# Kernel optimization log

Hardware: AMD Instinct MI355X
Metric: run time of the kernel (lower is better)

The kernel has to match this reference:

```python
import jax, jax.numpy as jnp
import numpy as np

EPS = 1e-12
B, C, H, M, E, P = 2, 20000, 64, 8, 200000, 3


def setup_inputs() -> dict:
    key = jax.random.key(0)
    ks = jax.random.split(key, 24)
    inp = {}
    inp["features"] = jax.random.normal(ks[0], (B, C, H), jnp.float32)
    inp["positions"] = jax.random.normal(ks[1], (B, C, P), jnp.float32)
    inp["edge_index"] = jax.random.randint(ks[2], (2, E), 0, C)
    inp["degree"] = jax.random.randint(ks[3], (C,), 1, 33).astype(jnp.float32)
    inp["cell_node_indices"] = jax.random.randint(ks[4], (C, M), 0, C)
    mask = (jax.random.uniform(ks[5], (C, M)) > 0.3).astype(jnp.float32)
    inp["cell_node_mask"] = mask.at[:, 0].set(1.0)  # first node always valid (pad semantics)

    def lin(k, fan_in, fan_out):
        return (jax.random.normal(k, (fan_in, fan_out), jnp.float32) / np.sqrt(fan_in)).astype(jnp.float32)

    # message MLP: Linear(2H+4 -> H), SiLU, Linear(H -> H)
    inp["W1"] = lin(ks[6], 2 * H + 4, H); inp["b1"] = jnp.zeros((H,), jnp.float32)
    inp["W2"] = lin(ks[7], H, H);         inp["b2"] = jnp.zeros((H,), jnp.float32)
    # position MLP: Linear(H -> H), SiLU, Linear(H -> 1)
    inp["P1"] = lin(ks[8], H, H);  inp["pb1"] = jnp.zeros((H,), jnp.float32)
    inp["P2"] = lin(ks[9], H, 1);  inp["pb2"] = jnp.zeros((1,), jnp.float32)
    # update MLP: Linear(2H -> H), SiLU, Linear(H -> H)
    inp["U1"] = lin(ks[10], 2 * H, H); inp["ub1"] = jnp.zeros((H,), jnp.float32)
    inp["U2"] = lin(ks[11], H, H);     inp["ub2"] = jnp.zeros((H,), jnp.float32)
    return inp


def _mlp(x, Wa, ba, Wb, bb):
    return jax.nn.silu(x @ Wa + ba) @ Wb + bb


def _forward(features, positions, edge_index, degree, cell_node_indices, cell_node_mask,
             W1, b1, W2, b2, P1, pb1, P2, pb2, U1, ub1, U2, ub2):
    src, dst = edge_index[0], edge_index[1]
    # gather padded node positions per cell: [B, C, M, P]
    node_pos = positions[:, cell_node_indices]

    h_src = features[:, src]                      # [B,E,H]
    h_dst = features[:, dst]
    rel = positions[:, src] - positions[:, dst]   # [B,E,P]
    dist = jnp.linalg.norm(rel, axis=-1, keepdims=True)  # [B,E,1]

    sp = node_pos[:, src]                         # [B,E,M,P]
    dp = node_pos[:, dst]
    mx = cell_node_mask[src]                      # [E,M]
    my = cell_node_mask[dst]

    # pairwise distances [B,E,M,M] via gram trick (avoids [B,E,M,M,P] intermediate)
    sp2 = jnp.sum(sp * sp, -1)                    # [B,E,M]
    dp2 = jnp.sum(dp * dp, -1)
    cross = jnp.einsum('bemp,benp->bemn', sp, dp)
    d = jnp.sqrt(jnp.maximum(sp2[..., :, None] + dp2[..., None, :] - 2.0 * cross, 0.0) + EPS)

    # masked pairwise-distance sum
    w = mx[:, :, None] * my[:, None, :]           # [E,M,M]
    pairwise = jnp.sum(d * w[None], axis=(-1, -2))  # [B,E]

    # centroid distance
    denx = jnp.maximum(mx.sum(-1, keepdims=True), EPS)  # [E,1]
    deny = jnp.maximum(my.sum(-1, keepdims=True), EPS)
    cx = jnp.sum(sp * mx[None, :, :, None], axis=2) / denx[None]  # [B,E,P]
    cy = jnp.sum(dp * my[None, :, :, None], axis=2) / deny[None]
    centroid = jnp.linalg.norm(cx - cy, axis=-1)  # [B,E]

    # Hausdorff distance (masked min/max)
    inf = jnp.float32(jnp.inf)
    d_xy = jnp.where(my[None, :, None, :] <= 0, inf, d)
    min_xy = jnp.where(mx[None] <= 0, 0.0, d_xy.min(-1))  # [B,E,M]
    h_xy = min_xy.max(-1)                                  # [B,E]
    d_yx = jnp.where(mx[None, :, None, :] <= 0, inf, jnp.swapaxes(d, -1, -2))
    min_yx = jnp.where(my[None] <= 0, 0.0, d_yx.min(-1))
    h_yx = min_yx.max(-1)
    haus = jnp.maximum(h_xy, h_yx)

    invariants = jnp.concatenate([dist, pairwise[..., None], centroid[..., None], haus[..., None]], -1)  # [B,E,4]
    msg_in = jnp.concatenate([h_src, h_dst, invariants], -1)  # [B,E,2H+4]
    messages = _mlp(msg_in, W1, b1, W2, b2)                   # [B,E,H]

    # scatter-aggregate into destination cells, degree-normalize
    agg = jnp.zeros_like(features).at[:, dst].add(messages)
    agg = agg / jnp.maximum(degree, 1.0)[None, :, None]

    # position update
    wts = jnp.tanh(_mlp(messages, P1, pb1, P2, pb2))          # [B,E,1]
    pos_upd = jnp.zeros_like(positions).at[:, dst].add(wts * rel)

    new_features = features + _mlp(jnp.concatenate([features, agg], -1), U1, ub1, U2, ub2)
    new_positions = positions + pos_upd
    return new_features, new_positions


def reference(features, positions, edge_index, degree, cell_node_indices, cell_node_mask,
              W1, b1, W2, b2, P1, pb1, P2, pb2, U1, ub1, U2, ub2):
    return _forward(features, positions, edge_index, degree, cell_node_indices, cell_node_mask,
                    W1, b1, W2, b2, P1, pb1, P2, pb2, U1, ub1, U2, ub2)
```

## Files before the change

### kernel.cpp

```cpp
#include <hip/hip_runtime.h>
#include <hip/hip_bf16.h>

#define B_ 2
#define C_ 20000
#define H_ 64
#define M_ 8
#define E_ 200000
#define P_ 3
#define EPS_ 1e-12f
#define ET_ (E_ / 64)

typedef __attribute__((ext_vector_type(8))) short short8;
typedef __attribute__((ext_vector_type(4))) float float4v;

__device__ __forceinline__ float rcp_(float x)  { return __builtin_amdgcn_rcpf(x); }
__device__ __forceinline__ float sqrt_(float x) { return __builtin_amdgcn_sqrtf(x); }
__device__ __forceinline__ float silu_(float x) {
    return x * __builtin_amdgcn_rcpf(1.f + __expf(-x));
}
__device__ __forceinline__ float tanh_(float x) {
    float e = __expf(2.f * x);
    return 1.f - 2.f * __builtin_amdgcn_rcpf(e + 1.f);
}
__device__ __forceinline__ unsigned short f2b(float f) {
    unsigned u = __float_as_uint(f);
    unsigned r = (u + 0x7FFF + ((u >> 16) & 1)) >> 16;
    return (unsigned short)r;
}
__device__ __forceinline__ float b2f(unsigned short h) {
    return __uint_as_float(((unsigned)h) << 16);
}
__device__ __forceinline__ unsigned pk2u(float a, float b) {
    __hip_bfloat162 h = __float22bfloat162_rn(make_float2(a, b));
    unsigned u; __builtin_memcpy(&u, &h, sizeof(u)); return u;
}
__device__ __forceinline__ float lo16f(unsigned u) { return __uint_as_float(u << 16); }
__device__ __forceinline__ float hi16f(unsigned u) { return __uint_as_float(u & 0xFFFF0000u); }

#define W1S_OFF 0
#define W2S_OFF 8192
#define P1S_OFF 12288
#define U1S_OFF 16384
#define U2S_OFF 24576
#define WBUF_ELEMS 28672

#define NB_PREP  120
#define NB_FEATB 2500
#define NB_DESC  157
#define NB_HIST  782
#define NB_ZAGG  2500
#define NB_PCOPY 118
#define NB_COMBO (NB_PREP + NB_FEATB + NB_DESC + NB_HIST + NB_ZAGG + NB_PCOPY)


__global__ __launch_bounds__(256) void combo_kernel(
    const float* __restrict__ W1, const float* __restrict__ W2,
    const float* __restrict__ P1, const float* __restrict__ U1,
    const float* __restrict__ U2, unsigned short* __restrict__ wbuf,
    const float* __restrict__ feat, unsigned short* __restrict__ featb,
    const float* __restrict__ pos, const int* __restrict__ cni,
    const float* __restrict__ mask, unsigned* __restrict__ descp,
    const int* __restrict__ ei, int* __restrict__ cnt,
    float* __restrict__ aggf, float* __restrict__ out_pos)
{
    const int bid = blockIdx.x;
    if (bid < NB_PREP) {
        int t = bid * 256 + threadIdx.x;
        if (t >= WBUF_ELEMS) return;
        const float* W; int e;
        if (t < W2S_OFF)      { W = W1; e = t; }
        else if (t < U1S_OFF) { W = (t < P1S_OFF) ? W2 : P1; e = (t < P1S_OFF) ? t - W2S_OFF : t - P1S_OFF; }
        else if (t < U2S_OFF) { W = U1; e = t - U1S_OFF; }
        else                  { W = U2; e = t - U2S_OFF; }
        int j = e & 7, lane = (e >> 3) & 63, nt = (e >> 9) & 3, kk = e >> 11;
        int k = kk * 32 + ((lane >> 4) * 8) + j;
        int n = nt * 16 + (lane & 15);
        wbuf[t] = f2b(W[k * 64 + n]);
    } else if (bid < NB_PREP + NB_FEATB) {
        int t = (bid - NB_PREP) * 256 + threadIdx.x;
        float4 v = *(const float4*)&feat[(size_t)t * 4];
        *(uint2*)&featb[(size_t)t * 4] = make_uint2(pk2u(v.x, v.y), pk2u(v.z, v.w));
    } else if (bid < NB_PREP + NB_FEATB + NB_DESC) {
        int tid = (bid - NB_PREP - NB_FEATB) * 256 + threadIdx.x;
        if (tid >= B_ * C_) return;
        int b = tid / C_, c = tid - b * C_;
        const float* pb = pos + (size_t)b * C_ * P_;
        unsigned* D = descp + (size_t)tid * 32;
        int4 n0 = *(const int4*)&cni[c*8];
        int4 n1 = *(const int4*)&cni[c*8 + 4];
        float4 m0 = *(const float4*)&mask[c*8];
        float4 m1 = *(const float4*)&mask[c*8 + 4];
        int ni[8] = {n0.x, n0.y, n0.z, n0.w, n1.x, n1.y, n1.z, n1.w};
        float mm[8] = {m0.x, m0.y, m0.z, m0.w, m1.x, m1.y, m1.z, m1.w};
        float sx = 0.f, sy = 0.f, sz = 0.f, sm = 0.f;
        #pragma unroll
        for (int m = 0; m < 8; ++m) {
            float x = pb[ni[m]*3+0], y = pb[ni[m]*3+1], z = pb[ni[m]*3+2];
            ((uint2*)D)[m] = make_uint2(pk2u(x, y), pk2u(z, mm[m]));
            sx += x * mm[m]; sy += y * mm[m]; sz += z * mm[m]; sm += mm[m];
        }
        float inv = rcp_(fmaxf(sm, EPS_));
        *(float4*)(D + 16) = make_float4(sx * inv, sy * inv, sz * inv, sm);
        *(float4*)(D + 20) = make_float4(pb[c*3+0], pb[c*3+1], pb[c*3+2], 0.f);
    } else if (bid < NB_PREP + NB_FEATB + NB_DESC + NB_HIST) {
        int e = (bid - NB_PREP - NB_FEATB - NB_DESC) * 256 + threadIdx.x;
        if (e >= E_) return;
        atomicAdd(&cnt[ei[E_ + e]], 1);
    } else if (bid < NB_PREP + NB_FEATB + NB_DESC + NB_HIST + NB_ZAGG) {
        int t = (bid - NB_PREP - NB_FEATB - NB_DESC - NB_HIST) * 256 + threadIdx.x;
        *(float4*)&aggf[(size_t)t * 4] = make_float4(0.f, 0.f, 0.f, 0.f);
    } else {
        int t = (bid - NB_PREP - NB_FEATB - NB_DESC - NB_HIST - NB_ZAGG) * 256 + threadIdx.x;
        if (t >= (B_ * C_ * P_) / 4) return;
        *(float4*)&out_pos[(size_t)t * 4] = *(const float4*)&pos[(size_t)t * 4];
    }
}

__global__ __launch_bounds__(256) void alloc_kernel(
    const int* __restrict__ cnt, int* __restrict__ cursor, int* __restrict__ total)
{
    int idx = blockIdx.x * 256 + threadIdx.x;
    int lane = threadIdx.x & 63;
    int v = (idx < C_) ? cnt[idx] : 0;
    int inc = v;
    #pragma unroll
    for (int s = 1; s < 64; s <<= 1) {
        int n = __shfl_up(inc, s);
        if (lane >= s) inc += n;
    }
    int wtot = __shfl(inc, 63);
    int base = 0;
    if (lane == 0) base = atomicAdd(total, wtot);
    base = __shfl(base, 0);
    if (idx < C_) cursor[idx] = base + inc - v;
}

__global__ __launch_bounds__(256) void scatter_kernel(
    const int* __restrict__ ei, int* __restrict__ cursor, int2* __restrict__ sed)
{
    int e = blockIdx.x * 256 + threadIdx.x;
    if (e >= E_) return;
    int s = ei[e], d = ei[E_ + e];
    int slot = atomicAdd(&cursor[d], 1);
    sed[slot] = make_int2(s, d);
}

__global__ __launch_bounds__(256) void geom_kernel(
    const int2* __restrict__ sed, const unsigned* __restrict__ descp,
    float4* __restrict__ ivA, float4* __restrict__ ivR)
{
    int idx = blockIdx.x * 256 + threadIdx.x;
    if (idx >= B_ * E_) return;
    int b = idx / E_, slot = idx - b * E_;
    int2 sd = sed[slot];
    const unsigned* Ds = descp + ((size_t)b * C_ + sd.x) * 32;
    const unsigned* Dd = descp + ((size_t)b * C_ + sd.y) * 32;

    uint2 spk[8], dpk[8];
    #pragma unroll
    for (int i = 0; i < 8; ++i) { spk[i] = ((const uint2*)Ds)[i]; dpk[i] = ((const uint2*)Dd)[i]; }
    float4 Sc = *(const float4*)(Ds + 16), Dc = *(const float4*)(Dd + 16);
    float4 Sp = *(const float4*)(Ds + 20), Dp = *(const float4*)(Dd + 20);

    const float INFV = __builtin_inff();
    float4 S[8]; float rowmin[8];
    #pragma unroll
    for (int i = 0; i < 8; ++i) {
        S[i] = make_float4(lo16f(spk[i].x), hi16f(spk[i].x),
                           lo16f(spk[i].y), hi16f(spk[i].y));
        rowmin[i] = INFV;
    }
    float pair = 0.f, hyx = 0.f;
    #pragma unroll
    for (int j = 0; j < 8; ++j) {
        float djx = lo16f(dpk[j].x), djy = hi16f(dpk[j].x);
        float djz = lo16f(dpk[j].y), djw = hi16f(dpk[j].y);
        float colmin = INFV;
        #pragma unroll
        for (int i = 0; i < 8; ++i) {
            float dx = S[i].x - djx, dy = S[i].y - djy, dz = S[i].z - djz;
            float dd = sqrt_(dx*dx + dy*dy + dz*dz + EPS_);
            pair += dd * S[i].w * djw;
            rowmin[i] = (djw    > 0.f) ? fminf(rowmin[i], dd) : rowmin[i];
            colmin    = (S[i].w > 0.f) ? fminf(colmin, dd)    : colmin;
        }
        hyx = fmaxf(hyx, (djw > 0.f) ? colmin : 0.f);
    }
    float hxy = 0.f;
    #pragma unroll
    for (int i = 0; i < 8; ++i)
        hxy = fmaxf(hxy, (S[i].w > 0.f) ? rowmin[i] : 0.f);
    float cdx = Sc.x - Dc.x, cdy = Sc.y - Dc.y, cdz = Sc.z - Dc.z;
    float rx = Sp.x - Dp.x, ry = Sp.y - Dp.y, rz = Sp.z - Dp.z;
    ivA[idx] = make_float4(sqrt_(rx*rx + ry*ry + rz*rz), pair,
                           sqrt_(cdx*cdx + cdy*cdy + cdz*cdz), fmaxf(hxy, hyx));
    ivR[idx] = make_float4(rx, ry, rz, 0.f);
}

__global__ __launch_bounds__(256, 8) void edge_kernel(
    const unsigned short* __restrict__ featb,
    const int2* __restrict__ sed,
    const float4* __restrict__ ivA, const float4* __restrict__ ivR,
    const unsigned short* __restrict__ wbuf, const float* __restrict__ W1,
    const float* __restrict__ b1, const float* __restrict__ b2,
    const float* __restrict__ pb1, const float* __restrict__ P2,
    const float* __restrict__ pb2,
    float* __restrict__ aggf, float* __restrict__ out_pos)
{
    __shared__ unsigned short lds[4 * 2304];

    const int tid  = threadIdx.x;
    const int w    = tid >> 6;
    const int lane = tid & 63;
    const int q    = lane >> 4;
    const int l16  = lane & 15;
    const int w16  = w * 16;

    const int bidr = blockIdx.x;
    const int xcd  = bidr & 7, kblk = bidr >> 3;
    const int qq   = (B_ * ET_) >> 3, rr_ = (B_ * ET_) & 7;
    const int tile = (xcd < rr_ ? xcd * (qq + 1) : rr_ * (qq + 1) + (xcd - rr_) * qq) + kblk;

    const int b    = tile / ET_;
    const int i0   = (tile - b * ET_) * 64;
    const unsigned short* fb = featb + (size_t)b * C_ * H_;

    float4 iva[4];
    #pragma unroll
    for (int i = 0; i < 4; ++i)
        iva[i] = ivA[(size_t)b * E_ + i0 + w16 + q*4 + i];
    const float4 relv = ivR[(size_t)b * E_ + i0 + w16 + l16];

    const int2 sd  = sed[i0 + lane];
    const int s_l  = sd.x;
    const int d_l  = sd.y;
    const int dg   = __shfl(d_l, w16 + l16);

    unsigned short* Xw = lds + w * 2304;
    unsigned short* Hw = Xw;
    unsigned short* Mw = Xw + 1152;

    const int rr4 = lane >> 4, c4 = lane & 15;
    #pragma unroll
    for (int it = 0; it < 4; ++it) {
        int rloc = it * 4 + rr4;
        int r = w16 + rloc;
        int sr = __shfl(s_l, r);
        int dr = __shfl(d_l, r);
        uint2 vs = *(const uint2*)&fb[(size_t)sr * 64 + c4 * 4];
        uint2 vd = *(const uint2*)&fb[(size_t)dr * 64 + c4 * 4];
        *(uint2*)&Xw[rloc*136 + c4*4]      = vs;
        *(uint2*)&Xw[rloc*136 + 64 + c4*4] = vd;
    }

    float4v acc[4];
    #pragma unroll
    for (int nt = 0; nt < 4; ++nt) {
        float bv = b1[nt*16 + l16];
        float wa = W1[128*64 + nt*16 + l16];
        float wb = W1[129*64 + nt*16 + l16];
        float wc = W1[130*64 + nt*16 + l16];
        float wd = W1[131*64 + nt*16 + l16];
        #pragma unroll
        for (int i = 0; i < 4; ++i)
            acc[nt][i] = bv + iva[i].x*wa + iva[i].y*wb
                            + iva[i].z*wc + iva[i].w*wd;
    }
    #pragma unroll
    for (int kk = 0; kk < 4; ++kk) {
        short8 a = *(const short8*)&Xw[l16*136 + kk*32 + q*8];
        #pragma unroll
        for (int nt = 0; nt < 4; ++nt) {
            short8 bf = *(const short8*)&wbuf[W1S_OFF + (((kk*4 + nt)*64) + lane) * 8];
            acc[nt] = __builtin_amdgcn_mfma_f32_16x16x32_bf16(a, bf, acc[nt], 0, 0, 0);
        }
    }
    #pragma unroll
    for (int nt = 0; nt < 4; ++nt)
        #pragma unroll
        for (int i = 0; i < 4; i += 2) {
            unsigned u = pk2u(silu_(acc[nt][i]), silu_(acc[nt][i+1]));
            Hw[(q*4 + i)*72     + nt*16 + l16] = (unsigned short)u;
            Hw[(q*4 + i + 1)*72 + nt*16 + l16] = (unsigned short)(u >> 16);
        }

    float4v mac[4];
    #pragma unroll
    for (int nt = 0; nt < 4; ++nt) {
        float bv = b2[nt*16 + l16];
        mac[nt] = (float4v){bv, bv, bv, bv};
    }
    #pragma unroll
    for (int kk = 0; kk < 2; ++kk) {
        short8 a = *(const short8*)&Hw[l16*72 + kk*32 + q*8];
        #pragma unroll
        for (int nt = 0; nt < 4; ++nt) {
            short8 bf = *(const short8*)&wbuf[W2S_OFF + (((kk*4 + nt)*64) + lane) * 8];
            mac[nt] = __builtin_amdgcn_mfma_f32_16x16x32_bf16(a, bf, mac[nt], 0, 0, 0);
        }
    }
    #pragma unroll
    for (int nt = 0; nt < 4; ++nt)
        #pragma unroll
        for (int i = 0; i < 4; i += 2) {
            unsigned u = pk2u(mac[nt][i], mac[nt][i+1]);
            Mw[(q*4 + i)*72     + nt*16 + l16] = (unsigned short)u;
            Mw[(q*4 + i + 1)*72 + nt*16 + l16] = (unsigned short)(u >> 16);
        }

    float4v gac[4];
    #pragma unroll
    for (int nt = 0; nt < 4; ++nt) {
        float bv = pb1[nt*16 + l16];
        gac[nt] = (float4v){bv, bv, bv, bv};
    }
    #pragma unroll
    for (int kk = 0; kk < 2; ++kk) {
        short8 a = *(const short8*)&Mw[l16*72 + kk*32 + q*8];
        #pragma unroll
        for (int nt = 0; nt < 4; ++nt) {
            short8 bf = *(const short8*)&wbuf[P1S_OFF + (((kk*4 + nt)*64) + lane) * 8];
            gac[nt] = __builtin_amdgcn_mfma_f32_16x16x32_bf16(a, bf, gac[nt], 0, 0, 0);
        }
    }
    float p2v[4];
    #pragma unroll
    for (int nt = 0; nt < 4; ++nt) p2v[nt] = P2[nt*16 + l16];
    const float pb2v = pb2[0];

    #pragma unroll
    for (int i = 0; i < 4; ++i) {
        float p = 0.f;
        #pragma unroll
        for (int nt = 0; nt < 4; ++nt) p += silu_(gac[nt][i]) * p2v[nt];
        p += __shfl_xor(p, 8);
        p += __shfl_xor(p, 4);
        p += __shfl_xor(p, 2);
        p += __shfl_xor(p, 1);
        float wt = tanh_(p + pb2v);
        if (l16 == 0) *(float*)&Mw[(q*4 + i)*72 + 64] = wt;
    }

    float mrow[16];
    #pragma unroll
    for (int rr = 0; rr < 16; ++rr) mrow[rr] = b2f(Mw[rr*72 + lane]);
    float wtl = *(const float*)&Mw[l16*72 + 64];

    float* aggB = aggf + (size_t)b * C_ * 64;
    float* opB  = out_pos + (size_t)b * C_ * 3;

    int dnx = __shfl(d_l, (lane + 1) & 63);
    bool bf64 = (lane == 63) || (d_l != dnx);
    unsigned long long bm64t = __ballot(bf64) & 0x7FFFFFFFFFFFFFFFull;

    unsigned mask16 = (unsigned)((bm64t >> w16) & 0xFFFFull) | 0x8000u;
    const bool head_true = (w16 > 0) && ((bm64t >> (w16 - 1)) & 1ull);

    unsigned below = mask16 & ((1u << l16) - 1u);
    int dist = l16 - (below ? (31 - __clz((int)below)) : -1) - 1;

    {
        float sx = wtl * relv.x, sy = wtl * relv.y, sz = wtl * relv.z;
        #pragma unroll
        for (int s = 1; s < 16; s <<= 1) {
            float tx = __shfl_up(sx, s);
            float ty = __shfl_up(sy, s);
            float tz = __shfl_up(sz, s);
            if (dist >= s) { sx += tx; sy += ty; sz += tz; }
        }
        bool bflag = (mask16 >> l16) & 1u;
        if (bflag && q == 0) {
            float* p = &opB[(size_t)dg * 3];
            atomicAdd(p + 0, sx);
            atomicAdd(p + 1, sy);
            atomicAdd(p + 2, sz);
        }
    }

    float colacc = 0.f;
    int prev = -1;
    #pragma unroll
    for (int rr = 0; rr < 16; ++rr) {
        colacc += mrow[rr];
        if (mask16 & (1u << rr)) {
            int dseg = __builtin_amdgcn_readlane(dg, rr);
            bool tend   = (bm64t >> (w16 + rr)) & 1ull;
            bool tstart = (prev >= 0) || head_true;
            if (tend && tstart)
                aggB[(size_t)dseg * 64 + lane] = colacc;
            else
                atomicAdd(&aggB[(size_t)dseg * 64 + lane], colacc);
            colacc = 0.f;
            prev = rr;
        }
    }
}

__global__ __launch_bounds__(256, 8) void node_kernel(
    const unsigned short* __restrict__ featb,
    const float* __restrict__ aggf, const float* __restrict__ deg,
    const unsigned short* __restrict__ wbuf,
    const float* __restrict__ ub1, const float* __restrict__ ub2,
    float* __restrict__ out_feat)
{
    __shared__ unsigned short lds[4 * 2304];

    const int tid  = threadIdx.x;
    const int w    = tid >> 6;
    const int lane = tid & 63;
    const int q    = lane >> 4;
    const int l16  = lane & 15;
    const int g0   = blockIdx.x * 64;

    unsigned short* Xw = lds + w * 2304;
    unsigned short* Hw = Xw;

    const int rr4 = lane >> 4, c4 = lane & 15;
    #pragma unroll
    for (int it = 0; it < 4; ++it) {
        int rloc = it * 4 + rr4;
        int g = g0 + w*16 + rloc;
        int gc = (g >= C_) ? g - C_ : g;
        float sc = rcp_(fmaxf(deg[gc], 1.f));
        uint2  vf = *(const uint2*)&featb[(size_t)g * 64 + c4 * 4];
        float4 va = *(const float4*)&aggf[(size_t)g * 64 + c4 * 4];
        *(uint2*)&Xw[rloc*136 + c4*4]      = vf;
        *(uint2*)&Xw[rloc*136 + 64 + c4*4] =
            make_uint2(pk2u(va.x*sc, va.y*sc), pk2u(va.z*sc, va.w*sc));
    }

    float4v acc[4];
    #pragma unroll
    for (int nt = 0; nt < 4; ++nt) {
        float bv = ub1[nt*16 + l16];
        acc[nt] = (float4v){bv, bv, bv, bv};
    }
    #pragma unroll
    for (int kk = 0; kk < 4; ++kk) {
        short8 a = *(const short8*)&Xw[l16*136 + kk*32 + q*8];
        #pragma unroll
        for (int nt = 0; nt < 4; ++nt) {
            short8 bf = *(const short8*)&wbuf[U1S_OFF + (((kk*4 + nt)*64) + lane) * 8];
            acc[nt] = __builtin_amdgcn_mfma_f32_16x16x32_bf16(a, bf, acc[nt], 0, 0, 0);
        }
    }
    #pragma unroll
    for (int nt = 0; nt < 4; ++nt)
        #pragma unroll
        for (int i = 0; i < 4; i += 2) {
            unsigned u = pk2u(silu_(acc[nt][i]), silu_(acc[nt][i+1]));
            Hw[(q*4 + i)*72     + nt*16 + l16] = (unsigned short)u;
            Hw[(q*4 + i + 1)*72 + nt*16 + l16] = (unsigned short)(u >> 16);
        }

    float4v oac[4];
    #pragma unroll
    for (int nt = 0; nt < 4; ++nt) {
        float bv = ub2[nt*16 + l16];
        oac[nt] = (float4v){bv, bv, bv, bv};
    }
    #pragma unroll
    for (int kk = 0; kk < 2; ++kk) {
        short8 a = *(const short8*)&Hw[l16*72 + kk*32 + q*8];
        #pragma unroll
        for (int nt = 0; nt < 4; ++nt) {
            short8 bf = *(const short8*)&wbuf[U2S_OFF + (((kk*4 + nt)*64) + lane) * 8];
            oac[nt] = __builtin_amdgcn_mfma_f32_16x16x32_bf16(a, bf, oac[nt], 0, 0, 0);
        }
    }
    #pragma unroll
    for (int nt = 0; nt < 4; ++nt)
        #pragma unroll
        for (int i = 0; i < 4; ++i) {
            size_t idx = (size_t)(g0 + w*16 + q*4 + i) * 64 + nt*16 + l16;
            out_feat[idx] = b2f(featb[idx]) + oac[nt][i];
        }
}

extern "C" void kernel_launch(void* const* d_in, const int* in_sizes, int n_in,
                              void* d_out, int out_size, void* d_ws, size_t ws_size,
                              hipStream_t stream) {
    const float* feat = (const float*)d_in[0];
    const float* pos  = (const float*)d_in[1];
    const int*   ei   = (const int*)d_in[2];
    const float* deg  = (const float*)d_in[3];
    const int*   cni  = (const int*)d_in[4];
    const float* mask = (const float*)d_in[5];
    const float* W1   = (const float*)d_in[6];
    const float* b1   = (const float*)d_in[7];
    const float* W2   = (const float*)d_in[8];
    const float* b2   = (const float*)d_in[9];
    const float* P1   = (const float*)d_in[10];
    const float* pb1  = (const float*)d_in[11];
    const float* P2   = (const float*)d_in[12];
    const float* pb2  = (const float*)d_in[13];
    const float* U1   = (const float*)d_in[14];
    const float* ub1  = (const float*)d_in[15];
    const float* U2   = (const float*)d_in[16];
    const float* ub2  = (const float*)d_in[17];

    float* out_feat = (float*)d_out;
    float* out_pos  = out_feat + (size_t)B_ * C_ * H_;

    unsigned* descp = (unsigned*)d_ws;
    float*  aggf = (float*)(descp + (size_t)B_ * C_ * 32);
    float4* ivA  = (float4*)(aggf + (size_t)B_ * C_ * 64);
    float4* ivR  = ivA + (size_t)B_ * E_;
    unsigned short* featb = (unsigned short*)(ivR + (size_t)B_ * E_);
    unsigned short* wbuf  = featb + (size_t)B_ * C_ * 64;
    int* cnt    = (int*)(wbuf + WBUF_ELEMS);
    int* total  = cnt + C_;
    int* cursor = total + 1;
    int2* sed   = (int2*)(cursor + C_ + 1);

    hipMemsetAsync(cnt, 0, (C_ + 1) * sizeof(int), stream);

    combo_kernel<<<NB_COMBO, 256, 0, stream>>>(
        W1, W2, P1, U1, U2, wbuf, feat, featb, pos, cni, mask, descp, ei, cnt,
        aggf, out_pos);

    alloc_kernel<<<(C_ + 255) / 256, 256, 0, stream>>>(cnt, cursor, total);

    scatter_kernel<<<(E_ + 255) / 256, 256, 0, stream>>>(ei, cursor, sed);

    geom_kernel<<<(B_ * E_ + 255) / 256, 256, 0, stream>>>(sed, descp, ivA, ivR);

    edge_kernel<<<B_ * ET_, 256, 0, stream>>>(
        featb, sed, ivA, ivR, wbuf, W1, b1, b2, pb1, P2, pb2, aggf, out_pos);

    node_kernel<<<(B_ * C_) / 64, 256, 0, stream>>>(
        featb, aggf, deg, wbuf, ub1, ub2, out_feat);
}
```

Baseline: 213.8 us.

## Fuse geometric invariant computation into edge kernel with 4-way lane split

Drops the separate geom_kernel and computes the per-edge geometric invariants (distance, pairwise sum, centroid distance, Hausdorff) inside edge_kernel. Each of the 4 lane groups handles 2 of the 8 destination nodes, and the partial results are combined with xor shuffles. This removes one launch and the write and re-read of the ivA/ivR intermediates. In exchange it adds register pressure to an edge kernel launched with bounds (256,8), which may cause spills or lower occupancy.

```diff
diff --git a/kernel.cpp b/kernel.cpp
--- a/kernel.cpp
+++ b/kernel.cpp
@@ -145,62 +145,10 @@
     sed[slot] = make_int2(s, d);
 }
 
-__global__ __launch_bounds__(256) void geom_kernel(
-    const int2* __restrict__ sed, const unsigned* __restrict__ descp,
-    float4* __restrict__ ivA, float4* __restrict__ ivR)
-{
-    int idx = blockIdx.x * 256 + threadIdx.x;
-    if (idx >= B_ * E_) return;
-    int b = idx / E_, slot = idx - b * E_;
-    int2 sd = sed[slot];
-    const unsigned* Ds = descp + ((size_t)b * C_ + sd.x) * 32;
-    const unsigned* Dd = descp + ((size_t)b * C_ + sd.y) * 32;
-
-    uint2 spk[8], dpk[8];
-    #pragma unroll
-    for (int i = 0; i < 8; ++i) { spk[i] = ((const uint2*)Ds)[i]; dpk[i] = ((const uint2*)Dd)[i]; }
-    float4 Sc = *(const float4*)(Ds + 16), Dc = *(const float4*)(Dd + 16);
-    float4 Sp = *(const float4*)(Ds + 20), Dp = *(const float4*)(Dd + 20);
-
-    const float INFV = __builtin_inff();
-    float4 S[8]; float rowmin[8];
-    #pragma unroll
-    for (int i = 0; i < 8; ++i) {
-        S[i] = make_float4(lo16f(spk[i].x), hi16f(spk[i].x),
-                           lo16f(spk[i].y), hi16f(spk[i].y));
-        rowmin[i] = INFV;
-    }
-    float pair = 0.f, hyx = 0.f;
-    #pragma unroll
-    for (int j = 0; j < 8; ++j) {
-        float djx = lo16f(dpk[j].x), djy = hi16f(dpk[j].x);
-        float djz = lo16f(dpk[j].y), djw = hi16f(dpk[j].y);
-        float colmin = INFV;
-        #pragma unroll
-        for (int i = 0; i < 8; ++i) {
-            float dx = S[i].x - djx, dy = S[i].y - djy, dz = S[i].z - djz;
-            float dd = sqrt_(dx*dx + dy*dy + dz*dz + EPS_);
-            pair += dd * S[i].w * djw;
-            rowmin[i] = (djw    > 0.f) ? fminf(rowmin[i], dd) : rowmin[i];
-            colmin    = (S[i].w > 0.f) ? fminf(colmin, dd)    : colmin;
-        }
-        hyx = fmaxf(hyx, (djw > 0.f) ? colmin : 0.f);
-    }
-    float hxy = 0.f;
-    #pragma unroll
-    for (int i = 0; i < 8; ++i)
-        hxy = fmaxf(hxy, (S[i].w > 0.f) ? rowmin[i] : 0.f);
-    float cdx = Sc.x - Dc.x, cdy = Sc.y - Dc.y, cdz = Sc.z - Dc.z;
-    float rx = Sp.x - Dp.x, ry = Sp.y - Dp.y, rz = Sp.z - Dp.z;
-    ivA[idx] = make_float4(sqrt_(rx*rx + ry*ry + rz*rz), pair,
-                           sqrt_(cdx*cdx + cdy*cdy + cdz*cdz), fmaxf(hxy, hyx));
-    ivR[idx] = make_float4(rx, ry, rz, 0.f);
-}
-
 __global__ __launch_bounds__(256, 8) void edge_kernel(
     const unsigned short* __restrict__ featb,
     const int2* __restrict__ sed,
-    const float4* __restrict__ ivA, const float4* __restrict__ ivR,
+    const unsigned* __restrict__ descp,
     const unsigned short* __restrict__ wbuf, const float* __restrict__ W1,
     const float* __restrict__ b1, const float* __restrict__ b2,
     const float* __restrict__ pb1, const float* __restrict__ P2,
@@ -225,20 +173,76 @@
     const int i0   = (tile - b * ET_) * 64;
     const unsigned short* fb = featb + (size_t)b * C_ * H_;
 
-    float4 iva[4];
-    #pragma unroll
-    for (int i = 0; i < 4; ++i)
-        iva[i] = ivA[(size_t)b * E_ + i0 + w16 + q*4 + i];
-    const float4 relv = ivR[(size_t)b * E_ + i0 + w16 + l16];
-
     const int2 sd  = sed[i0 + lane];
     const int s_l  = sd.x;
     const int d_l  = sd.y;
+    const int sg   = __shfl(s_l, w16 + l16);
     const int dg   = __shfl(d_l, w16 + l16);
 
     unsigned short* Xw = lds + w * 2304;
     unsigned short* Hw = Xw;
     unsigned short* Mw = Xw + 1152;
+
+    const unsigned* Ds = descp + ((size_t)b * C_ + sg) * 32;
+    const unsigned* Dd = descp + ((size_t)b * C_ + dg) * 32;
+    uint2 spk[8];
+    #pragma unroll
+    for (int i = 0; i < 8; ++i) spk[i] = ((const uint2*)Ds)[i];
+    uint2 dpk[2];
+    dpk[0] = ((const uint2*)Dd)[q*2 + 0];
+    dpk[1] = ((const uint2*)Dd)[q*2 + 1];
+    float4 Sc = *(const float4*)(Ds + 16), Dc = *(const float4*)(Dd + 16);
+    float4 Sp = *(const float4*)(Ds + 20), Dp = *(const float4*)(Dd + 20);
+
+    const float INFV = __builtin_inff();
+    float4 S[8]; float rowmin[8];
+    #pragma unroll
+    for (int i = 0; i < 8; ++i) {
+        S[i] = make_float4(lo16f(spk[i].x), hi16f(spk[i].x),
+                           lo16f(spk[i].y), hi16f(spk[i].y));
+        rowmin[i] = INFV;
+    }
+    float pair = 0.f, hyx = 0.f;
+    #pragma unroll
+    for (int jj = 0; jj < 2; ++jj) {
+        float djx = lo16f(dpk[jj].x), djy = hi16f(dpk[jj].x);
+        float djz = lo16f(dpk[jj].y), djw = hi16f(dpk[jj].y);
+        float colmin = INFV;
+        #pragma unroll
+        for (int i = 0; i < 8; ++i) {
+            float dx = S[i].x - djx, dy = S[i].y - djy, dz = S[i].z - djz;
+            float dd = sqrt_(dx*dx + dy*dy + dz*dz + EPS_);
+            pair += dd * S[i].w * djw;
+            rowmin[i] = (djw    > 0.f) ? fminf(rowmin[i], dd) : rowmin[i];
+            colmin    = (S[i].w > 0.f) ? fminf(colmin, dd)    : colmin;
+        }
+        hyx = fmaxf(hyx, (djw > 0.f) ? colmin : 0.f);
+    }
+    pair += __shfl_xor(pair, 16);  pair += __shfl_xor(pair, 32);
+    hyx = fmaxf(hyx, __shfl_xor(hyx, 16));  hyx = fmaxf(hyx, __shfl_xor(hyx, 32));
+    #pragma unroll
+    for (int i = 0; i < 8; ++i) {
+        rowmin[i] = fminf(rowmin[i], __shfl_xor(rowmin[i], 16));
+        rowmin[i] = fminf(rowmin[i], __shfl_xor(rowmin[i], 32));
+    }
+    float hxy = 0.f;
+    #pragma unroll
+    for (int i = 0; i < 8; ++i)
+        hxy = fmaxf(hxy, (S[i].w > 0.f) ? rowmin[i] : 0.f);
+    float cdx = Sc.x - Dc.x, cdy = Sc.y - Dc.y, cdz = Sc.z - Dc.z;
+    const float relx = Sp.x - Dp.x, rely = Sp.y - Dp.y, relz = Sp.z - Dp.z;
+    const float ivx = sqrt_(relx*relx + rely*rely + relz*relz);
+    const float ivy = pair;
+    const float ivz = sqrt_(cdx*cdx + cdy*cdy + cdz*cdz);
+    const float ivw = fmaxf(hxy, hyx);
+
+    float4 iva[4];
+    #pragma unroll
+    for (int i = 0; i < 4; ++i) {
+        int r = q*4 + i;
+        iva[i] = make_float4(__shfl(ivx, r), __shfl(ivy, r),
+                             __shfl(ivz, r), __shfl(ivw, r));
+    }
 
     const int rr4 = lane >> 4, c4 = lane & 15;
     #pragma unroll
@@ -360,7 +364,7 @@
     int dist = l16 - (below ? (31 - __clz((int)below)) : -1) - 1;
 
     {
-        float sx = wtl * relv.x, sy = wtl * relv.y, sz = wtl * relv.z;
+        float sx = wtl * relx, sy = wtl * rely, sz = wtl * relz;
         #pragma unroll
         for (int s = 1; s < 16; s <<= 1) {
             float tx = __shfl_up(sx, s);
@@ -504,9 +508,7 @@
 
     unsigned* descp = (unsigned*)d_ws;
     float*  aggf = (float*)(descp + (size_t)B_ * C_ * 32);
-    float4* ivA  = (float4*)(aggf + (size_t)B_ * C_ * 64);
-    float4* ivR  = ivA + (size_t)B_ * E_;
-    unsigned short* featb = (unsigned short*)(ivR + (size_t)B_ * E_);
+    unsigned short* featb = (unsigned short*)(aggf + (size_t)B_ * C_ * 64);
     unsigned short* wbuf  = featb + (size_t)B_ * C_ * 64;
     int* cnt    = (int*)(wbuf + WBUF_ELEMS);
     int* total  = cnt + C_;
@@ -523,10 +525,8 @@
 
     scatter_kernel<<<(E_ + 255) / 256, 256, 0, stream>>>(ei, cursor, sed);
 
-    geom_kernel<<<(B_ * E_ + 255) / 256, 256, 0, stream>>>(sed, descp, ivA, ivR);
-
     edge_kernel<<<B_ * ET_, 256, 0, stream>>>(
-        featb, sed, ivA, ivR, wbuf, W1, b1, b2, pb1, P2, pb2, aggf, out_pos);
+        featb, sed, descp, wbuf, W1, b1, b2, pb1, P2, pb2, aggf, out_pos);
 
     node_kernel<<<(B_ * C_) / 64, 256, 0, stream>>>(
         featb, aggf, deg, wbuf, ub1, ub2, out_feat);
```

New measurement: 211.6 us (median of 2 runs). No clear change (-1.0%).
